# Kernel optimization log

Measured on AMD Instinct MI355X. Metric: run time of the kernel, lower is better.

The kernel has to match this reference:

```python
import jax, jax.numpy as jnp
import numpy as np

NUM_STATES = 64
HIDDEN = 32
NUM_ACTIONS = 3
SEQ_LEN = 512
BATCH = 2048


def setup_inputs() -> dict:
    key = jax.random.key(0)
    ks = jax.random.split(key, 7)
    s_ih = 1.0 / np.sqrt(HIDDEN)
    x = jax.random.normal(ks[0], (SEQ_LEN, BATCH, NUM_STATES), dtype=jnp.float32)
    # PyTorch LSTM params: gate order [i, f, g, o], each block of size HIDDEN
    W_ih = jax.random.uniform(ks[1], (4 * HIDDEN, NUM_STATES), minval=-s_ih, maxval=s_ih, dtype=jnp.float32)
    W_hh = jax.random.uniform(ks[2], (4 * HIDDEN, HIDDEN), minval=-s_ih, maxval=s_ih, dtype=jnp.float32)
    b_ih = jax.random.uniform(ks[3], (4 * HIDDEN,), minval=-s_ih, maxval=s_ih, dtype=jnp.float32)
    b_hh = jax.random.uniform(ks[4], (4 * HIDDEN,), minval=-s_ih, maxval=s_ih, dtype=jnp.float32)
    s_d = 1.0 / np.sqrt(HIDDEN)
    W_d = jax.random.uniform(ks[5], (NUM_ACTIONS, HIDDEN), minval=-s_d, maxval=s_d, dtype=jnp.float32)
    b_d = jax.random.uniform(ks[6], (NUM_ACTIONS,), minval=-s_d, maxval=s_d, dtype=jnp.float32)
    return {"x": x, "W_ih": W_ih, "W_hh": W_hh, "b_ih": b_ih, "b_hh": b_hh, "W_d": W_d, "b_d": b_d}


def _lstm_last_hidden(x, W_ih, W_hh, b_ih, b_hh):
    # x: [T, B, F] time-major, as in nn.LSTM(batch_first=False)
    B = x.shape[1]
    H = W_hh.shape[1]
    # Precompute input projections for all timesteps in one GEMM: [T, B, 4H]
    x_proj = jnp.einsum('tbf,gf->tbg', x, W_ih) + (b_ih + b_hh)

    def step(carry, xp_t):
        h, c = carry
        gates = xp_t + h @ W_hh.T  # [B, 4H]
        i, f, g, o = jnp.split(gates, 4, axis=-1)
        i = jax.nn.sigmoid(i)
        f = jax.nn.sigmoid(f)
        g = jnp.tanh(g)
        o = jax.nn.sigmoid(o)
        c = f * c + i * g
        h = o * jnp.tanh(c)
        return (h, c), None

    h0 = jnp.zeros((B, H), dtype=x.dtype)
    c0 = jnp.zeros((B, H), dtype=x.dtype)
    (h_T, _), _ = jax.lax.scan(step, (h0, c0), x_proj)
    return h_T  # [B, H] == lstm output at last timestep (x[-1,:,:])


def reference(x, W_ih, W_hh, b_ih, b_hh, W_d, b_d):
    h_T = _lstm_last_hidden(x, W_ih, W_hh, b_ih, b_hh)
    h = jax.nn.relu(h_T)
    return h @ W_d.T + b_d  # [B, num_actions]
```

## Files before the change

kernel.cpp:

```cpp
#include <hip/hip_runtime.h>

typedef __bf16 bf16_t;
typedef __bf16 bf16x8 __attribute__((ext_vector_type(8)));
typedef __bf16 bf16x4 __attribute__((ext_vector_type(4)));
typedef float  f32x4  __attribute__((ext_vector_type(4)));

#define T_STEPS 512
#define BATCH   2048
#define NS      64
#define HID     32
#define HSTR    40
#define FSTR    36

__device__ __forceinline__ float fast_sigmoid(float x) {
  return __builtin_amdgcn_rcpf(1.0f + __builtin_amdgcn_exp2f(-1.4426950408889634f * x));
}
__device__ __forceinline__ float fast_tanh(float x) {
  return 1.0f - 2.0f * __builtin_amdgcn_rcpf(1.0f + __builtin_amdgcn_exp2f(2.8853900817779268f * x));
}

__device__ __forceinline__ void barrier_lgkm() {
  asm volatile("s_waitcnt lgkmcnt(0)\n\ts_barrier" ::: "memory");
}

#define MFMA(A, B, C) __builtin_amdgcn_mfma_f32_16x16x32_bf16((A), (B), (C), 0, 0, 0)

__global__ __launch_bounds__(128, 1)
void lstm_policy_kernel(const float* __restrict__ x,
                        const float* __restrict__ W_ih,
                        const float* __restrict__ W_hh,
                        const float* __restrict__ b_ih,
                        const float* __restrict__ b_hh,
                        const float* __restrict__ W_d,
                        const float* __restrict__ b_d,
                        float* __restrict__ out)
{
  __shared__ bf16_t hbuf[2][16 * HSTR];
  __shared__ float  hf[16 * FSTR];

  const int tid  = threadIdx.x;
  const int wave = tid >> 6;
  const int lane = tid & 63;
  const int m    = lane & 15;
  const int q    = lane >> 4;
  const int u0   = wave << 4;
  const int row0 = blockIdx.x << 4;

  for (int i = tid; i < 16 * HSTR; i += 128) hbuf[0][i] = (bf16_t)0.0f;

  bf16x8 a_ih[4][2], a_hh[4];
  f32x4  bias[4];
  #pragma unroll
  for (int G = 0; G < 4; ++G) {
    const int wrow = (G << 5) + u0 + m;
    const float* pih = W_ih + wrow * 64;
    const float* phh = W_hh + (wrow << 5);
    #pragma unroll
    for (int j = 0; j < 8; ++j) {
      a_ih[G][0][j] = (bf16_t)pih[(q << 3) + j];
      a_ih[G][1][j] = (bf16_t)pih[32 + (q << 3) + j];
      a_hh[G][j]    = (bf16_t)phh[(q << 3) + j];
    }
    #pragma unroll
    for (int r = 0; r < 4; ++r) {
      const int u = (G << 5) + u0 + (q << 2) + r;
      bias[G][r] = b_ih[u] + b_hh[u];
    }
  }

  const size_t xstep = (size_t)BATCH * NS;
  const float* xb = x + (size_t)row0 * NS;
  const int    lo = m * NS + (q << 3);

  f32x4 xf[4][4];
  {
    const float* p1 = xb + 1 * xstep + lo;
    const float* p2 = xb + 2 * xstep + lo;
    const float* p3 = xb + 3 * xstep + lo;
    const float* p4 = xb + 4 * xstep + lo;
    xf[1][0]=*(const f32x4*)(p1); xf[1][1]=*(const f32x4*)(p1+4); xf[1][2]=*(const f32x4*)(p1+32); xf[1][3]=*(const f32x4*)(p1+36);
    xf[2][0]=*(const f32x4*)(p2); xf[2][1]=*(const f32x4*)(p2+4); xf[2][2]=*(const f32x4*)(p2+32); xf[2][3]=*(const f32x4*)(p2+36);
    xf[3][0]=*(const f32x4*)(p3); xf[3][1]=*(const f32x4*)(p3+4); xf[3][2]=*(const f32x4*)(p3+32); xf[3][3]=*(const f32x4*)(p3+36);
    xf[0][0]=*(const f32x4*)(p4); xf[0][1]=*(const f32x4*)(p4+4); xf[0][2]=*(const f32x4*)(p4+32); xf[0][3]=*(const f32x4*)(p4+36);
  }

  f32x4 acc[2][4];
  {
    const float* p0 = xb + lo;
    f32x4 x0a = *(const f32x4*)(p0), x0b = *(const f32x4*)(p0 + 4);
    f32x4 x0c = *(const f32x4*)(p0 + 32), x0d = *(const f32x4*)(p0 + 36);
    bf16x8 xA, xB;
    #pragma unroll
    for (int j = 0; j < 4; ++j) {
      xA[j] = (bf16_t)x0a[j]; xA[4+j] = (bf16_t)x0b[j];
      xB[j] = (bf16_t)x0c[j]; xB[4+j] = (bf16_t)x0d[j];
    }
    #pragma unroll
    for (int G = 0; G < 4; ++G) {
      acc[0][G] = MFMA(a_ih[G][0], xA, bias[G]);
      acc[0][G] = MFMA(a_ih[G][1], xB, acc[0][G]);
    }
  }

  float cst[4] = {0.0f, 0.0f, 0.0f, 0.0f};

  __syncthreads();

  #define STEP(P)                                                                     \
  do {                                                                                \
    const int tt = t + (P);                                                           \
                                 \
    const bf16x8 hfr = *(const bf16x8*)(&hbuf[(P) & 1][m * HSTR + (q << 3)]);         \
            \
    {                                                                                 \
      bf16x8 xA, xB;                                                                  \
      _Pragma("unroll")                                                               \
      for (int j = 0; j < 4; ++j) {                                                   \
        xA[j]   = (bf16_t)xf[((P)+1)&3][0][j]; xA[4+j] = (bf16_t)xf[((P)+1)&3][1][j]; \
        xB[j]   = (bf16_t)xf[((P)+1)&3][2][j]; xB[4+j] = (bf16_t)xf[((P)+1)&3][3][j]; \
      }                                                                               \
      _Pragma("unroll")                                                               \
      for (int G = 0; G < 4; ++G) {                                                   \
        acc[((P)+1)&1][G] = MFMA(a_ih[G][0], xA, bias[G]);                            \
        acc[((P)+1)&1][G] = MFMA(a_ih[G][1], xB, acc[((P)+1)&1][G]);                  \
      }                                                                               \
      int tp = tt + 5; if (tp > T_STEPS - 1) tp = T_STEPS - 1;                        \
      const float* pf = xb + (size_t)tp * xstep + lo;                                 \
      xf[((P)+1)&3][0] = *(const f32x4*)(pf);                                         \
      xf[((P)+1)&3][1] = *(const f32x4*)(pf + 4);                                     \
      xf[((P)+1)&3][2] = *(const f32x4*)(pf + 32);                                    \
      xf[((P)+1)&3][3] = *(const f32x4*)(pf + 36);                                    \
    }                                                                                 \
                               \
    f32x4 gi = MFMA(a_hh[0], hfr, acc[(P)&1][0]);                                     \
    f32x4 gf = MFMA(a_hh[1], hfr, acc[(P)&1][1]);                                     \
    f32x4 gg = MFMA(a_hh[2], hfr, acc[(P)&1][2]);                                     \
    f32x4 go = MFMA(a_hh[3], hfr, acc[(P)&1][3]);                                     \
    bf16x4 hv;                                                                        \
    _Pragma("unroll")                                                                 \
    for (int r = 0; r < 4; ++r) {                                                     \
      const float ig  = fast_sigmoid(gi[r]);                                          \
      const float fg  = fast_sigmoid(gf[r]);                                          \
      const float gv  = fast_tanh(gg[r]);                                             \
      const float og  = fast_sigmoid(go[r]);                                          \
      const float og2 = og + og;                              \
      const float cn  = __builtin_fmaf(fg, cst[r], ig * gv);                          \
      cst[r] = cn;                                                                    \
           \
      const float rr  = __builtin_amdgcn_rcpf(1.0f +                                  \
                          __builtin_amdgcn_exp2f(2.8853900817779268f * cn));          \
      const float h   = __builtin_fmaf(-og2, rr, og);                                 \
      hv[r] = (bf16_t)h;                                                              \
      if (tt == T_STEPS - 1) hf[m * FSTR + u0 + (q << 2) + r] = fmaxf(h, 0.0f);       \
    }                                                                                 \
    *(bf16x4*)(&hbuf[((P)&1)^1][m * HSTR + u0 + (q << 2)]) = hv;                      \
    barrier_lgkm();                                                                   \
  } while (0)

  #pragma unroll 1
  for (int t = 0; t < T_STEPS; t += 4) {
    STEP(0);
    STEP(1);
    STEP(2);
    STEP(3);
  }
  #undef STEP

  __syncthreads();

  if (tid < 48) {
    const int r = tid / 3;
    const int a = tid - r * 3;
    float s = b_d[a];
    #pragma unroll
    for (int u = 0; u < HID; ++u)
      s += hf[r * FSTR + u] * W_d[a * HID + u];
    out[(size_t)(row0 + r) * 3 + a] = s;
  }
}

extern "C" void kernel_launch(void* const* d_in, const int* in_sizes, int n_in,
                              void* d_out, int out_size, void* d_ws, size_t ws_size,
                              hipStream_t stream) {
  const float* x    = (const float*)d_in[0];
  const float* W_ih = (const float*)d_in[1];
  const float* W_hh = (const float*)d_in[2];
  const float* b_ih = (const float*)d_in[3];
  const float* b_hh = (const float*)d_in[4];
  const float* W_d  = (const float*)d_in[5];
  const float* b_d  = (const float*)d_in[6];
  float* out = (float*)d_out;

  dim3 grid(BATCH / 16);
  dim3 block(128);
  hipLaunchKernelGGL(lstm_policy_kernel, grid, block, 0, stream,
                     x, W_ih, W_hh, b_ih, b_hh, W_d, b_d, out);
}
```

Measured before the change: 499.1 us.

## Use one wave per batch tile and keep hidden state in registers

```diff
diff --git a/kernel.cpp b/kernel.cpp
--- a/kernel.cpp
+++ b/kernel.cpp
@@ -2,30 +2,19 @@
 
 typedef __bf16 bf16_t;
 typedef __bf16 bf16x8 __attribute__((ext_vector_type(8)));
-typedef __bf16 bf16x4 __attribute__((ext_vector_type(4)));
 typedef float  f32x4  __attribute__((ext_vector_type(4)));
 
 #define T_STEPS 512
 #define BATCH   2048
 #define NS      64
-#define HID     32
-#define HSTR    40
 #define FSTR    36
 
-__device__ __forceinline__ float fast_sigmoid(float x) {
-  return __builtin_amdgcn_rcpf(1.0f + __builtin_amdgcn_exp2f(-1.4426950408889634f * x));
-}
-__device__ __forceinline__ float fast_tanh(float x) {
-  return 1.0f - 2.0f * __builtin_amdgcn_rcpf(1.0f + __builtin_amdgcn_exp2f(2.8853900817779268f * x));
-}
-
-__device__ __forceinline__ void barrier_lgkm() {
-  asm volatile("s_waitcnt lgkmcnt(0)\n\ts_barrier" ::: "memory");
-}
+#define K_SIG  (-1.4426950408889634f)
+#define K_TANH ( 2.8853900817779268f)
 
 #define MFMA(A, B, C) __builtin_amdgcn_mfma_f32_16x16x32_bf16((A), (B), (C), 0, 0, 0)
 
-__global__ __launch_bounds__(128, 1)
+__global__ __launch_bounds__(64, 1)
 void lstm_policy_kernel(const float* __restrict__ x,
                         const float* __restrict__ W_ih,
                         const float* __restrict__ W_hh,
@@ -35,36 +24,35 @@
                         const float* __restrict__ b_d,
                         float* __restrict__ out)
 {
-  __shared__ bf16_t hbuf[2][16 * HSTR];
-  __shared__ float  hf[16 * FSTR];
+  __shared__ float hf[16 * FSTR];
 
-  const int tid  = threadIdx.x;
-  const int wave = tid >> 6;
-  const int lane = tid & 63;
+  const int lane = threadIdx.x;
   const int m    = lane & 15;
   const int q    = lane >> 4;
-  const int u0   = wave << 4;
   const int row0 = blockIdx.x << 4;
 
-  for (int i = tid; i < 16 * HSTR; i += 128) hbuf[0][i] = (bf16_t)0.0f;
-
-  bf16x8 a_ih[4][2], a_hh[4];
-  f32x4  bias[4];
+  bf16x8 a_ih[4][2][2], a_hh[4][2];
+  f32x4  bias[4][2];
   #pragma unroll
   for (int G = 0; G < 4; ++G) {
-    const int wrow = (G << 5) + u0 + m;
-    const float* pih = W_ih + wrow * 64;
-    const float* phh = W_hh + (wrow << 5);
+    const float k = (G == 2) ? K_TANH : K_SIG;
     #pragma unroll
-    for (int j = 0; j < 8; ++j) {
-      a_ih[G][0][j] = (bf16_t)pih[(q << 3) + j];
-      a_ih[G][1][j] = (bf16_t)pih[32 + (q << 3) + j];
-      a_hh[G][j]    = (bf16_t)phh[(q << 3) + j];
-    }
-    #pragma unroll
-    for (int r = 0; r < 4; ++r) {
-      const int u = (G << 5) + u0 + (q << 2) + r;
-      bias[G][r] = b_ih[u] + b_hh[u];
+    for (int U = 0; U < 2; ++U) {
+      const int wrow = (G << 5) + (U << 4) + m;
+      const float* pih = W_ih + wrow * 64;
+      const float* phh = W_hh + (wrow << 5);
+      #pragma unroll
+      for (int j = 0; j < 8; ++j) {
+        a_ih[G][U][0][j] = (bf16_t)(k * pih[(q << 3) + j]);
+        a_ih[G][U][1][j] = (bf16_t)(k * pih[32 + (q << 3) + j]);
+        const int us = (j < 4) ? ((q << 2) + j) : (16 + (q << 2) + (j - 4));
+        a_hh[G][U][j] = (bf16_t)(k * phh[us]);
+      }
+      #pragma unroll
+      for (int r = 0; r < 4; ++r) {
+        const int u = (G << 5) + (U << 4) + (q << 2) + r;
+        bias[G][U][r] = (b_ih[u] + b_hh[u]) * k;
+      }
     }
   }
 
@@ -84,10 +72,10 @@
     xf[0][0]=*(const f32x4*)(p4); xf[0][1]=*(const f32x4*)(p4+4); xf[0][2]=*(const f32x4*)(p4+32); xf[0][3]=*(const f32x4*)(p4+36);
   }
 
-  f32x4 acc[2][4];
+  f32x4 acc[2][4][2];
   {
     const float* p0 = xb + lo;
-    f32x4 x0a = *(const f32x4*)(p0), x0b = *(const f32x4*)(p0 + 4);
+    f32x4 x0a = *(const f32x4*)(p0),      x0b = *(const f32x4*)(p0 + 4);
     f32x4 x0c = *(const f32x4*)(p0 + 32), x0d = *(const f32x4*)(p0 + 36);
     bf16x8 xA, xB;
     #pragma unroll
@@ -96,65 +84,68 @@
       xB[j] = (bf16_t)x0c[j]; xB[4+j] = (bf16_t)x0d[j];
     }
     #pragma unroll
-    for (int G = 0; G < 4; ++G) {
-      acc[0][G] = MFMA(a_ih[G][0], xA, bias[G]);
-      acc[0][G] = MFMA(a_ih[G][1], xB, acc[0][G]);
-    }
+    for (int G = 0; G < 4; ++G)
+      #pragma unroll
+      for (int U = 0; U < 2; ++U) {
+        acc[0][G][U] = MFMA(a_ih[G][U][0], xA, bias[G][U]);
+        acc[0][G][U] = MFMA(a_ih[G][U][1], xB, acc[0][G][U]);
+      }
   }
 
-  float cst[4] = {0.0f, 0.0f, 0.0f, 0.0f};
-
-  __syncthreads();
+  float cst[2][4] = {{0,0,0,0},{0,0,0,0}};
+  bf16x8 hB = {};
 
   #define STEP(P)                                                                     \
   do {                                                                                \
     const int tt = t + (P);                                                           \
-                                 \
-    const bf16x8 hfr = *(const bf16x8*)(&hbuf[(P) & 1][m * HSTR + (q << 3)]);         \
-            \
+    const int par = (P) & 1;                                                          \
+    f32x4 gr[4][2];                                                                   \
+    _Pragma("unroll")                                                                 \
+    for (int G = 0; G < 4; ++G)                                                       \
+      _Pragma("unroll")                                                               \
+      for (int U = 0; U < 2; ++U)                                                     \
+        gr[G][U] = MFMA(a_hh[G][U], hB, acc[par][G][U]);                              \
+                           \
     {                                                                                 \
+      const int ns = ((P) + 1) & 3;                                                   \
       bf16x8 xA, xB;                                                                  \
       _Pragma("unroll")                                                               \
       for (int j = 0; j < 4; ++j) {                                                   \
-        xA[j]   = (bf16_t)xf[((P)+1)&3][0][j]; xA[4+j] = (bf16_t)xf[((P)+1)&3][1][j]; \
-        xB[j]   = (bf16_t)xf[((P)+1)&3][2][j]; xB[4+j] = (bf16_t)xf[((P)+1)&3][3][j]; \
+        xA[j] = (bf16_t)xf[ns][0][j]; xA[4+j] = (bf16_t)xf[ns][1][j];                 \
+        xB[j] = (bf16_t)xf[ns][2][j]; xB[4+j] = (bf16_t)xf[ns][3][j];                 \
       }                                                                               \
       _Pragma("unroll")                                                               \
-      for (int G = 0; G < 4; ++G) {                                                   \
-        acc[((P)+1)&1][G] = MFMA(a_ih[G][0], xA, bias[G]);                            \
-        acc[((P)+1)&1][G] = MFMA(a_ih[G][1], xB, acc[((P)+1)&1][G]);                  \
-      }                                                                               \
+      for (int G = 0; G < 4; ++G)                                                     \
+        _Pragma("unroll")                                                             \
+        for (int U = 0; U < 2; ++U) {                                                 \
+          acc[par ^ 1][G][U] = MFMA(a_ih[G][U][0], xA, bias[G][U]);                   \
+          acc[par ^ 1][G][U] = MFMA(a_ih[G][U][1], xB, acc[par ^ 1][G][U]);           \
+        }                                                                             \
       int tp = tt + 5; if (tp > T_STEPS - 1) tp = T_STEPS - 1;                        \
       const float* pf = xb + (size_t)tp * xstep + lo;                                 \
-      xf[((P)+1)&3][0] = *(const f32x4*)(pf);                                         \
-      xf[((P)+1)&3][1] = *(const f32x4*)(pf + 4);                                     \
-      xf[((P)+1)&3][2] = *(const f32x4*)(pf + 32);                                    \
-      xf[((P)+1)&3][3] = *(const f32x4*)(pf + 36);                                    \
+      xf[ns][0] = *(const f32x4*)(pf);                                                \
+      xf[ns][1] = *(const f32x4*)(pf + 4);                                            \
+      xf[ns][2] = *(const f32x4*)(pf + 32);                                           \
+      xf[ns][3] = *(const f32x4*)(pf + 36);                                           \
     }                                                                                 \
-                               \
-    f32x4 gi = MFMA(a_hh[0], hfr, acc[(P)&1][0]);                                     \
-    f32x4 gf = MFMA(a_hh[1], hfr, acc[(P)&1][1]);                                     \
-    f32x4 gg = MFMA(a_hh[2], hfr, acc[(P)&1][2]);                                     \
-    f32x4 go = MFMA(a_hh[3], hfr, acc[(P)&1][3]);                                     \
-    bf16x4 hv;                                                                        \
+                  \
     _Pragma("unroll")                                                                 \
-    for (int r = 0; r < 4; ++r) {                                                     \
-      const float ig  = fast_sigmoid(gi[r]);                                          \
-      const float fg  = fast_sigmoid(gf[r]);                                          \
-      const float gv  = fast_tanh(gg[r]);                                             \
-      const float og  = fast_sigmoid(go[r]);                                          \
-      const float og2 = og + og;                              \
-      const float cn  = __builtin_fmaf(fg, cst[r], ig * gv);                          \
-      cst[r] = cn;                                                                    \
-           \
-      const float rr  = __builtin_amdgcn_rcpf(1.0f +                                  \
-                          __builtin_amdgcn_exp2f(2.8853900817779268f * cn));          \
-      const float h   = __builtin_fmaf(-og2, rr, og);                                 \
-      hv[r] = (bf16_t)h;                                                              \
-      if (tt == T_STEPS - 1) hf[m * FSTR + u0 + (q << 2) + r] = fmaxf(h, 0.0f);       \
-    }                                                                                 \
-    *(bf16x4*)(&hbuf[((P)&1)^1][m * HSTR + u0 + (q << 2)]) = hv;                      \
-    barrier_lgkm();                                                                   \
+    for (int U = 0; U < 2; ++U)                                                       \
+      _Pragma("unroll")                                                               \
+      for (int r = 0; r < 4; ++r) {                                                   \
+        const float iv = __builtin_amdgcn_rcpf(1.0f + __builtin_amdgcn_exp2f(gr[0][U][r])); \
+        const float fv = __builtin_amdgcn_rcpf(1.0f + __builtin_amdgcn_exp2f(gr[1][U][r])); \
+        const float rg = __builtin_amdgcn_rcpf(1.0f + __builtin_amdgcn_exp2f(gr[2][U][r])); \
+        const float ov = __builtin_amdgcn_rcpf(1.0f + __builtin_amdgcn_exp2f(gr[3][U][r])); \
+        const float gs = __builtin_fmaf(-2.0f * K_TANH, rg, K_TANH);   \
+        const float cn = __builtin_fmaf(fv, cst[U][r], iv * gs);        \
+        cst[U][r] = cn;                                                               \
+        const float rh  = __builtin_amdgcn_rcpf(1.0f + __builtin_amdgcn_exp2f(cn));   \
+        const float ov2 = ov + ov;                                                    \
+        const float h   = __builtin_fmaf(-ov2, rh, ov);                \
+        hB[(U << 2) + r] = (bf16_t)h;                                                 \
+        if (tt == T_STEPS - 1) hf[m * FSTR + (U << 4) + (q << 2) + r] = fmaxf(h, 0.0f); \
+      }                                                                               \
   } while (0)
 
   #pragma unroll 1
@@ -168,13 +159,13 @@
 
   __syncthreads();
 
-  if (tid < 48) {
-    const int r = tid / 3;
-    const int a = tid - r * 3;
+  if (lane < 48) {
+    const int r = lane / 3;
+    const int a = lane - r * 3;
     float s = b_d[a];
     #pragma unroll
-    for (int u = 0; u < HID; ++u)
-      s += hf[r * FSTR + u] * W_d[a * HID + u];
+    for (int u = 0; u < 32; ++u)
+      s += hf[r * FSTR + u] * W_d[a * 32 + u];
     out[(size_t)(row0 + r) * 3 + a] = s;
   }
 }
@@ -192,7 +183,7 @@
   float* out = (float*)d_out;
 
   dim3 grid(BATCH / 16);
-  dim3 block(128);
+  dim3 block(64);
   hipLaunchKernelGGL(lstm_policy_kernel, grid, block, 0, stream,
                      x, W_ih, W_hh, b_ih, b_hh, W_d, b_d, out);
 }
```

After: 605.1 us. 21.2% more time.
